# Performance work log

Hardware: AMD Instinct MI355X
Metric: run time of the kernel (lower is better)

Reference implementation:

```python
import jax, jax.numpy as jnp
import numpy as np

S = 17          # number of segment ids (0 = background, skipped)
MIN_H = 100.0   # HomographySmoothLoss.min_segment_pixels
MIN_V = 50.0    # ObjectVarianceLoss.min_segment_pixels
SUPPRESS = 0.1  # BoundaryAwareSmoothLoss.boundary_suppress


def _maxpool3(x):
    # torch F.max_pool2d(k=3, stride=1, pad=1) pads with -inf
    return jax.lax.reduce_window(x, -jnp.inf, jax.lax.max,
                                 (1, 1, 3, 3), (1, 1, 1, 1),
                                 ((0, 0), (0, 0), (1, 1), (1, 1)))


def _boundary_map(masks):
    lab = masks.astype(jnp.float32)[:, None]  # (B,1,H,W)
    dil = _maxpool3(lab)
    ero = -_maxpool3(-lab)
    return (dil != ero).astype(jnp.float32)


def _nearest(x, Ho, Wo):
    # torch F.interpolate(mode='nearest'): src = floor(dst * in/out)
    H, W = x.shape[-2], x.shape[-1]
    yi = (jnp.arange(Ho) * H) // Ho
    xi = (jnp.arange(Wo) * W) // Wo
    return x[..., yi, :][..., :, xi]


def _conv3(x, k):
    return jax.lax.conv_general_dilated(x, k, (1, 1), ((1, 1), (1, 1)),
                                        dimension_numbers=('NCHW', 'OIHW', 'NCHW'))


def _segment_losses(flow, masks):
    # Vectorized replacement of per-(batch,segment) python loops:
    # accumulate per-segment moments with segment_sum, then batched 3x3
    # normal-equation solves (equivalent to torch.lstsq affine fit).
    B, _, H, W = flow.shape
    NS = B * S
    xs = jnp.broadcast_to(jnp.arange(W, dtype=jnp.float32)[None, None, :], (B, H, W)).reshape(-1)
    ys = jnp.broadcast_to(jnp.arange(H, dtype=jnp.float32)[None, :, None], (B, H, W)).reshape(-1)
    u = flow[:, 0].reshape(-1)
    v = flow[:, 1].reshape(-1)
    seg = masks.reshape(-1)
    bidx = jnp.repeat(jnp.arange(B, dtype=jnp.int32), H * W)
    idx = bidx * S + seg                                  # global segment id
    ones = jnp.ones_like(xs)
    feats = jnp.stack([ones, xs, ys, xs * xs, xs * ys, ys * ys,
                       u, v, u * u, v * v, xs * u, ys * u, xs * v, ys * v], axis=1)
    sums = jax.ops.segment_sum(feats, idx, num_segments=NS)  # (NS,14)
    (n, Sx, Sy, Sxx, Sxy, Syy, Su, Sv, Suu, Svv,
     Sxu, Syu, Sxv, Syv) = [sums[:, i] for i in range(14)]
    segids = jnp.tile(jnp.arange(S), B)

    # ---- homography loss: per-segment affine least-squares fit ----
    valid_h = (segids != 0) & (n >= MIN_H)
    ATA = jnp.stack([jnp.stack([Sxx, Sxy, Sx], -1),
                     jnp.stack([Sxy, Syy, Sy], -1),
                     jnp.stack([Sx, Sy, n], -1)], axis=1)   # (NS,3,3)
    eye3 = jnp.eye(3, dtype=flow.dtype)
    ATA = jnp.where(valid_h[:, None, None], ATA, eye3)      # keep solve nonsingular
    ATb = jnp.stack([jnp.stack([Sxu, Sxv], -1),
                     jnp.stack([Syu, Syv], -1),
                     jnp.stack([Su, Sv], -1)], axis=1)      # (NS,3,2)
    ATb = jnp.where(valid_h[:, None, None], ATb, 0.0)
    params = jnp.linalg.solve(ATA, ATb)                     # (NS,3,2): [a,b,c] for u and v
    p = params[idx]                                         # (BHW,3,2) gather per pixel
    pred_u = xs * p[:, 0, 0] + ys * p[:, 1, 0] + p[:, 2, 0]
    pred_v = xs * p[:, 0, 1] + ys * p[:, 1, 1] + p[:, 2, 1]
    res = jnp.sqrt((u - pred_u) ** 2 + (v - pred_v) ** 2)
    res_mean = jax.ops.segment_sum(res, idx, num_segments=NS) / jnp.maximum(n, 1.0)
    nh = jnp.maximum(jnp.sum(valid_h), 1)
    homog = jnp.sum(res_mean * valid_h) / nh

    # ---- object variance loss (unbiased var, matches torch .var()) ----
    valid_v = (segids != 0) & (n >= MIN_V)
    nsafe = jnp.maximum(n, 2.0)
    var_u = (Suu - Su * Su / nsafe) / (nsafe - 1.0)
    var_v = (Svv - Sv * Sv / nsafe) / (nsafe - 1.0)
    nv = jnp.maximum(jnp.sum(valid_v), 1)
    ovar = jnp.sum((var_u + var_v) * valid_v) / nv
    return homog, ovar


def setup_inputs():
    key = jax.random.key(0)
    k1, k2, k3 = jax.random.split(key, 3)
    B, H, W = 8, 512, 1024
    flow = jax.random.normal(k1, (B, 2, H, W), jnp.float32)
    masks = jax.random.randint(k2, (B, H, W), 0, S).astype(jnp.int32)
    images = jax.random.uniform(k3, (B, 3, H, W), jnp.float32)
    return {"flow": flow, "masks": masks, "images": images}


def reference(flow, masks, images):
    boundary = _boundary_map(masks)                         # (B,1,H,W)
    homog, ovar = _segment_losses(flow, masks)

    # ---- boundary sharpness (sobel on flow magnitude) ----
    sobel_x = jnp.array([[-1., 0., 1.], [-2., 0., 2.], [-1., 0., 1.]], jnp.float32).reshape(1, 1, 3, 3)
    sobel_y = jnp.array([[-1., -2., -1.], [0., 0., 0.], [1., 2., 1.]], jnp.float32).reshape(1, 1, 3, 3)
    flow_mag = jnp.sqrt(jnp.sum(flow ** 2, axis=1, keepdims=True))
    fg = jnp.abs(_conv3(flow_mag, sobel_x)) + jnp.abs(_conv3(flow_mag, sobel_y))
    fg = fg / (jnp.max(fg) + 1e-6)
    bn = boundary / (jnp.max(boundary) + 1e-6)
    sharp = jnp.mean(bn * (1.0 - fg))

    # ---- boundary-aware edge-weighted smoothness ----
    flow_dx = flow[:, :, :, 1:] - flow[:, :, :, :-1]
    flow_dy = flow[:, :, 1:, :] - flow[:, :, :-1, :]
    g = jnp.mean(images, axis=1, keepdims=True)
    wx = jnp.exp(-jnp.abs(g[:, :, :, 1:] - g[:, :, :, :-1]) * 10.0)
    wy = jnp.exp(-jnp.abs(g[:, :, 1:, :] - g[:, :, :-1, :]) * 10.0)
    bx = _nearest(boundary, wx.shape[2], wx.shape[3])
    by = _nearest(boundary, wy.shape[2], wy.shape[3])
    wx = wx * (1.0 - (1.0 - SUPPRESS) * bx)
    wy = wy * (1.0 - (1.0 - SUPPRESS) * by)
    smooth = jnp.mean(jnp.abs(flow_dx) * wx) + jnp.mean(jnp.abs(flow_dy) * wy)

    # weights all 1.0; order: homography, boundary_sharpness, object_variance, boundary_smooth
    return jnp.stack([homog, sharp, ovar, smooth])
```

## Files before the change

kernel.cpp:

```cpp
#include <hip/hip_runtime.h>
#include <math.h>

#define BB 8
#define HH 512
#define WW 1024
#define HW (HH * WW)
#define NPIX (BB * HW)
#define NSEG 16
#define SUPPRESS 0.1f


__device__ __forceinline__ float wave_sum(float t) {
    #pragma unroll
    for (int off = 32; off > 0; off >>= 1) t += __shfl_down(t, off);
    return t;
}

#define REP8(M) M(0) M(1) M(2) M(3) M(4) M(5) M(6) M(7)


__device__ void moments_body(
    const float* __restrict__ flow, const int* __restrict__ masks,
    double* __restrict__ moments4, float* bins, int bid)
{
    const int tid  = threadIdx.x;
    const int lane = tid & 63;
    const int wid  = tid >> 6;
    const int colg = bid & 15;
    const int rowg = (bid >> 4) & 7;
    const int b    = bid >> 7;
    const int par  = bid & 3;

    const int c0 = colg * 64;
    const int r0 = rowg * 64;

    const float* fu = flow + (long long)b * (2LL * HW);
    const float* fv = fu + HW;
    const int*   mk = masks + (long long)b * HW;
    const int*   mrow = mk + r0 * WW + c0 + lane;
    const float* urow = fu + r0 * WW + c0 + lane;
    const float* vrow = fv + r0 * WW + c0 + lane;

    for (int i = tid; i < 2496; i += 256)
        *(float4*)&bins[i * 4] = make_float4(0.f, 0.f, 0.f, 0.f);
    __syncthreads();

    int   m0 = mrow[0];
    float u0 = urow[0], v0 = vrow[0];
    int   m1 = mrow[WW];
    float u1 = urow[WW], v1 = vrow[WW];

#define MPROC(RR, MM, UU, VV) { \
    const float y = (float)(r0 + (RR)); \
    float* bp = &bins[(MM) * 576 + lane]; \
    if (wid == 0) { \
        float b0 = bp[0], b1 = bp[64], b2 = bp[128]; \
        b0 += 1.f; b1 += y; b2 = fmaf(y, y, b2); \
        bp[0] = b0; bp[64] = b1; bp[128] = b2; \
    } else if (wid == 1) { \
        float b3 = bp[192], b5 = bp[320]; \
        b3 += (UU); b5 = fmaf((UU), (UU), b5); \
        bp[192] = b3; bp[320] = b5; \
    } else if (wid == 2) { \
        float b4 = bp[256], b6 = bp[384]; \
        b4 += (VV); b6 = fmaf((VV), (VV), b6); \
        bp[256] = b4; bp[384] = b6; \
    } else { \
        float b7 = bp[448], b8 = bp[512]; \
        b7 = fmaf(y, (UU), b7); b8 = fmaf(y, (VV), b8); \
        bp[448] = b7; bp[512] = b8; \
    } }

    #pragma unroll 1
    for (int r = 0; r < 64; r += 2) {
        const int o2 = ((r + 2) & 63) * WW;
        const int o3 = ((r + 3) & 63) * WW;
        const int   m2 = mrow[o2];
        const float u2 = urow[o2], v2 = vrow[o2];
        const int   m3 = mrow[o3];
        const float u3 = urow[o3], v3 = vrow[o3];

        MPROC(r, m0, u0, v0)
        MPROC(r + 1, m1, u1, v1)

        m0 = m2; u0 = u2; v0 = v2;
        m1 = m3; u1 = u3; v1 = v3;
    }
    __syncthreads();

    const unsigned long long SRC = 0x84736543210100ULL;
    const unsigned long long PW  = 0x01010000012010ULL;
    double* cell = moments4 + par * 1792 + b * 224;
    {
        const int p   = tid;
        const int act = (p < 224);
        const int pc  = act ? p : 0;
        const int segm = pc / 14;
        const int feat = pc - segm * 14;
        const int srcb = (int)((SRC >> (4 * feat)) & 15);
        const int pw   = (int)((PW  >> (4 * feat)) & 15);
        const float* bp = &bins[(segm + 1) * 576 + srcb * 64];
        float acc = 0.f;
        #pragma unroll 8
        for (int l0 = 0; l0 < 64; ++l0) {
            const int l = (l0 + lane) & 63;
            const float xv = (float)(c0 + l);
            const float w = (pw == 0) ? 1.f : ((pw == 1) ? xv : xv * xv);
            acc = fmaf(bp[l], w, acc);
        }
        if (act) atomicAdd(&cell[segm * 14 + feat], (double)acc);
    }
}

__device__ void stencil_body(
    const float* __restrict__ flow, const int* __restrict__ masks,
    const float* __restrict__ images,
    double* __restrict__ scal64, unsigned* __restrict__ maxfg64,
    char* smem, int bid)
{
    float    (*smX)[260] = (float (*)[260])(smem);
    float    (*smW)[260] = (float (*)[260])(smem + 4160);
    unsigned (*mX)[260]  = (unsigned (*)[260])(smem + 8320);
    unsigned (*mW)[260]  = (unsigned (*)[260])(smem + 12480);
    float    (*gX)[260]  = (float (*)[260])(smem + 16640);
    float    (*ue)[260]  = (float (*)[260])(smem + 18720);
    float    (*ve)[260]  = (float (*)[260])(smem + 20800);
    float    (*wred)[5]  = (float (*)[5])(smem + 22880);

    const int tid = threadIdx.x;
    const int lane = tid & 63;
    const long long base = (long long)bid * 2048;
    const int b  = (int)(base >> 19);
    const int h0 = (int)((base & (HW - 1)) >> 10);

    const float* fu = flow + (long long)b * (2LL * HW);
    const float* fv = fu + HW;
    const int*   mk = masks + (long long)b * HW;
    const float* i0 = images + (long long)b * (3LL * HW);
    const float* i1 = i0 + HW;
    const float* i2 = i1 + HW;

    const int c4 = tid * 4;
    float4 m4a[4];
    unsigned mbp[4];
    float4 ur[3], vr[3];
    float4 gr[3];

    #pragma unroll
    for (int r = 0; r < 4; ++r) {
        const int grow = h0 - 1 + r;
        const int mr = grow < 0 ? 0 : (grow > HH - 1 ? HH - 1 : grow);
        const int4 mv = *(const int4*)&mk[mr * WW + c4];
        mbp[r] = (unsigned)(mv.x & 255) | ((unsigned)(mv.y & 255) << 8) |
                 ((unsigned)(mv.z & 255) << 16) | ((unsigned)(mv.w & 255) << 24);

        float4 u4 = make_float4(0.f, 0.f, 0.f, 0.f);
        float4 v4 = make_float4(0.f, 0.f, 0.f, 0.f);
        if (grow >= 0 && grow <= HH - 1) {
            u4 = *(const float4*)&fu[grow * WW + c4];
            v4 = *(const float4*)&fv[grow * WW + c4];
        }
        float4 m4;
        m4.x = sqrtf(u4.x * u4.x + v4.x * v4.x);
        m4.y = sqrtf(u4.y * u4.y + v4.y * v4.y);
        m4.z = sqrtf(u4.z * u4.z + v4.z * v4.z);
        m4.w = sqrtf(u4.w * u4.w + v4.w * v4.w);
        m4a[r] = m4;
        smX[r][tid] = m4.x;
        smW[r][tid + 1] = m4.w;
        mX[r][tid] = (unsigned)(mv.x & 255);
        mW[r][tid + 1] = (unsigned)(mv.w & 255);
        if (tid == 0)   { smW[r][0] = 0.f;   mW[r][0] = (unsigned)(mv.x & 255); }
        if (tid == 255) { smX[r][256] = 0.f; mX[r][256] = (unsigned)(mv.w & 255); }
        if (r >= 1) { ur[r - 1] = u4; vr[r - 1] = v4; }
    }
    #pragma unroll
    for (int r = 0; r < 3; ++r) {
        const int grow = h0 + r;
        float4 g4 = make_float4(0.f, 0.f, 0.f, 0.f);
        if (grow <= HH - 1) {
            const float4 a  = *(const float4*)&i0[grow * WW + c4];
            const float4 bq = *(const float4*)&i1[grow * WW + c4];
            const float4 c  = *(const float4*)&i2[grow * WW + c4];
            g4.x = (a.x + bq.x + c.x) * (1.f / 3.f);
            g4.y = (a.y + bq.y + c.y) * (1.f / 3.f);
            g4.z = (a.z + bq.z + c.z) * (1.f / 3.f);
            g4.w = (a.w + bq.w + c.w) * (1.f / 3.f);
        }
        gr[r] = g4;
        if (r < 2) gX[r][tid] = g4.x;
    }
    ue[0][tid] = ur[0].x; ve[0][tid] = vr[0].x;
    ue[1][tid] = ur[1].x; ve[1][tid] = vr[1].x;
    __syncthreads();

    float a_dx = 0.f, a_dy = 0.f, a_sb = 0.f, a_sbf = 0.f, mfg = 0.f;

    #pragma unroll
    for (int lr = 0; lr < 2; ++lr) {
        const int h = h0 + lr;
        float a[3][6];
        unsigned long long kw[3];
        #pragma unroll
        for (int r = 0; r < 3; ++r) {
            const int rr = lr + r;
            const float4 own = m4a[rr];
            a[r][0] = smW[rr][tid];
            a[r][1] = own.x; a[r][2] = own.y; a[r][3] = own.z; a[r][4] = own.w;
            a[r][5] = smX[rr][tid + 1];
            kw[r] = (unsigned long long)mW[rr][tid]
                  | ((unsigned long long)mbp[rr] << 8)
                  | ((unsigned long long)mX[rr][tid + 1] << 40);
        }
        const float4 gc = gr[lr];
        const float4 gd4 = gr[lr + 1];
        const float gval[5] = {gc.x, gc.y, gc.z, gc.w, gX[lr][tid + 1]};
        const float gd[4]  = {gd4.x, gd4.y, gd4.z, gd4.w};
        const float4 uc4 = ur[lr],  vc4 = vr[lr];
        const float4 ud4 = ur[lr + 1], vd4 = vr[lr + 1];
        const float uc[5] = {uc4.x, uc4.y, uc4.z, uc4.w, ue[lr][tid + 1]};
        const float vc[5] = {vc4.x, vc4.y, vc4.z, vc4.w, ve[lr][tid + 1]};
        const float ud[4] = {ud4.x, ud4.y, ud4.z, ud4.w};
        const float vd[4] = {vd4.x, vd4.y, vd4.z, vd4.w};

        #pragma unroll
        for (int j = 0; j < 4; ++j) {
            const int w = c4 + j;
            const unsigned cseg = (unsigned)((kw[1] >> (8 * (j + 1))) & 255);
            int bnd = (((kw[0] >> (8 * j)) & 255) != cseg)
                    | (((kw[0] >> (8 * (j + 1))) & 255) != cseg)
                    | (((kw[0] >> (8 * (j + 2))) & 255) != cseg)
                    | (((kw[1] >> (8 * j)) & 255) != cseg)
                    | (((kw[1] >> (8 * (j + 2))) & 255) != cseg)
                    | (((kw[2] >> (8 * j)) & 255) != cseg)
                    | (((kw[2] >> (8 * (j + 1))) & 255) != cseg)
                    | (((kw[2] >> (8 * (j + 2))) & 255) != cseg);

            const float fgx = (a[0][j + 2] - a[0][j]) + 2.f * (a[1][j + 2] - a[1][j]) +
                              (a[2][j + 2] - a[2][j]);
            const float fgy = (a[2][j] + 2.f * a[2][j + 1] + a[2][j + 2]) -
                              (a[0][j] + 2.f * a[0][j + 1] + a[0][j + 2]);
            const float fgraw = fabsf(fgx) + fabsf(fgy);
            mfg = fmaxf(mfg, fgraw);
            if (bnd) { a_sb += 1.f; a_sbf += fgraw; }

            const float u = uc[j], v = vc[j], g0 = gval[j];
            if (w < WW - 1) {
                const float wgt = expf(-fabsf(gval[j + 1] - g0) * 10.f) * (bnd ? SUPPRESS : 1.f);
                a_dx += (fabsf(uc[j + 1] - u) + fabsf(vc[j + 1] - v)) * wgt;
            }
            if (h < HH - 1) {
                const float wgt = expf(-fabsf(gd[j] - g0) * 10.f) * (bnd ? SUPPRESS : 1.f);
                a_dy += (fabsf(ud[j] - u) + fabsf(vd[j] - v)) * wgt;
            }
        }
    }

    for (int off = 32; off > 0; off >>= 1) {
        a_dx += __shfl_down(a_dx, off);
        a_dy += __shfl_down(a_dy, off);
        a_sb += __shfl_down(a_sb, off);
        a_sbf += __shfl_down(a_sbf, off);
        mfg = fmaxf(mfg, __shfl_down(mfg, off));
    }
    if (lane == 0) {
        const int wv = tid >> 6;
        wred[wv][0] = a_dx; wred[wv][1] = a_dy; wred[wv][2] = a_sb;
        wred[wv][3] = a_sbf; wred[wv][4] = mfg;
    }
    __syncthreads();
    if (tid == 0) {
        float dx = 0.f, dy = 0.f, sb = 0.f, sbf = 0.f, mf = 0.f;
        for (int i = 0; i < 4; ++i) {
            dx += wred[i][0]; dy += wred[i][1]; sb += wred[i][2];
            sbf += wred[i][3]; mf = fmaxf(mf, wred[i][4]);
        }
        const int sl = bid & 63;
        atomicAdd(&scal64[sl * 4 + 0], (double)dx);
        atomicAdd(&scal64[sl * 4 + 1], (double)dy);
        atomicAdd(&scal64[sl * 4 + 2], (double)sb);
        atomicAdd(&scal64[sl * 4 + 3], (double)sbf);
        atomicMax(&maxfg64[sl], __float_as_uint(mf));
    }
}

__global__ __launch_bounds__(256) void uber_kernel(
    const float* __restrict__ flow,
    const int*   __restrict__ masks,
    const float* __restrict__ images,
    double* __restrict__ moments4,
    double* __restrict__ scal64,
    unsigned* __restrict__ maxfg64)
{
    __shared__ char smem[39936];
    const int bid = blockIdx.x;
    if ((bid % 3) == 2) {
        moments_body(flow, masks, moments4, (float*)smem, bid / 3);
    } else {
        stencil_body(flow, masks, images, scal64, maxfg64, smem,
                     (bid / 3) * 2 + (bid % 3));
    }
}

__global__ __launch_bounds__(128) void solve_kernel(
    const double* __restrict__ moments4,
    float* __restrict__ params,
    int* __restrict__ valid,
    float* __restrict__ out)
{
    const int i = threadIdx.x;
    double m[14];
    #pragma unroll
    for (int k = 0; k < 14; ++k) {
        double s = 0.0;
        #pragma unroll
        for (int par = 0; par < 4; ++par) s += moments4[par * 1792 + i * 14 + k];
        m[k] = s;
    }
    const double n = m[0];
    const int vh = (n >= 100.0) ? 1 : 0;
    float p[6] = {0.f, 0.f, 0.f, 0.f, 0.f, 0.f};
    if (vh) {
        double A[3][3] = {{m[3], m[4], m[1]},
                          {m[4], m[5], m[2]},
                          {m[1], m[2], n}};
        double Bm[3][2] = {{m[10], m[12]},
                           {m[11], m[13]},
                           {m[6],  m[7]}};
        for (int k = 0; k < 3; ++k) {
            int piv = k; double mx = fabs(A[k][k]);
            for (int r = k + 1; r < 3; ++r) {
                double a = fabs(A[r][k]);
                if (a > mx) { mx = a; piv = r; }
            }
            if (piv != k) {
                for (int c = 0; c < 3; ++c) { double t = A[k][c]; A[k][c] = A[piv][c]; A[piv][c] = t; }
                for (int c = 0; c < 2; ++c) { double t = Bm[k][c]; Bm[k][c] = Bm[piv][c]; Bm[piv][c] = t; }
            }
            const double inv = 1.0 / A[k][k];
            for (int r = k + 1; r < 3; ++r) {
                const double f = A[r][k] * inv;
                for (int c = k; c < 3; ++c) A[r][c] -= f * A[k][c];
                Bm[r][0] -= f * Bm[k][0];
                Bm[r][1] -= f * Bm[k][1];
            }
        }
        double X[3][2];
        for (int c = 0; c < 2; ++c) {
            X[2][c] = Bm[2][c] / A[2][2];
            X[1][c] = (Bm[1][c] - A[1][2] * X[2][c]) / A[1][1];
            X[0][c] = (Bm[0][c] - A[0][1] * X[1][c] - A[0][2] * X[2][c]) / A[0][0];
        }
        p[0] = (float)X[0][0]; p[1] = (float)X[1][0]; p[2] = (float)X[2][0];
        p[3] = (float)X[0][1]; p[4] = (float)X[1][1]; p[5] = (float)X[2][1];
    }
    valid[i] = vh;
    for (int c = 0; c < 6; ++c) params[i * 6 + c] = p[c];

    const int vv = (n >= 50.0) ? 1 : 0;
    double var = 0.0;
    if (vv) {
        const double ns = (n > 2.0) ? n : 2.0;
        const double var_u = (m[8] - m[6] * m[6] / ns) / (ns - 1.0);
        const double var_v = (m[9] - m[7] * m[7] / ns) / (ns - 1.0);
        var = var_u + var_v;
    }
    __shared__ double svar[128];
    __shared__ int scnt[128];
    svar[i] = var; scnt[i] = vv;
    __syncthreads();
    for (int s = 64; s > 0; s >>= 1) {
        if (i < s) { svar[i] += svar[i + s]; scnt[i] += scnt[i + s]; }
        __syncthreads();
    }
    if (i == 0) out[2] = (float)(svar[0] / (double)(scnt[0] > 1 ? scnt[0] : 1));
}

__global__ __launch_bounds__(256) void pass2_kernel(
    const float* __restrict__ flow,
    const int*   __restrict__ masks,
    const float* __restrict__ params,
    double* __restrict__ res4)
{
    __shared__ float sp[17 * 6];

    const long long base = (long long)blockIdx.x * 4096;
    const int b      = (int)(base >> 19);
    const int hwbase = (int)(base & (HW - 1));
    const int tid    = threadIdx.x;
    const int lane   = tid & 63;

    if (tid < 6) sp[tid] = 0.f;
    if (tid < 96) sp[6 + tid] = params[b * 96 + tid];
    __syncthreads();

    const float* fu = flow + (long long)b * (2LL * HW);
    const float* fv = fu + HW;
    const int*   mk = masks + (long long)b * HW;

#define DECLR(i) float r_##i = 0.f;
    REP8(DECLR)
#define DECLR2(i) float q_##i = 0.f;
    REP8(DECLR2)

    #pragma unroll
    for (int it = 0; it < 4; ++it) {
        const int i4 = hwbase + it * 1024 + tid * 4;
        const int4   m4 = *(const int4*)&mk[i4];
        const float4 u4 = *(const float4*)&fu[i4];
        const float4 v4 = *(const float4*)&fv[i4];
        const int segs[4] = {m4.x, m4.y, m4.z, m4.w};
        const float us[4] = {u4.x, u4.y, u4.z, u4.w};
        const float vs[4] = {v4.x, v4.y, v4.z, v4.w};
        #pragma unroll
        for (int j = 0; j < 4; ++j) {
            const int seg = segs[j];
            const float* pf = &sp[seg * 6];
            const int hw = i4 + j;
            const float x = (float)(hw & 1023), y = (float)((hw & (HW - 1)) >> 10);
            const float du = us[j] - (x * pf[0] + y * pf[1] + pf[2]);
            const float dv = vs[j] - (x * pf[3] + y * pf[4] + pf[5]);
            const float r = sqrtf(du * du + dv * dv);
            const int sr = seg - 1;
#define STEPR(i) r_##i += (sr == i) ? r : 0.f;
            REP8(STEPR)
#define STEPR2(i) q_##i += (sr == 8 + i) ? r : 0.f;
            REP8(STEPR2)
        }
    }

    const int par = blockIdx.x & 3;
    double* rb = &res4[par * 128 + b * 16];
#define FINR(i) { const float s = wave_sum(r_##i); \
    if (lane == 0) atomicAdd(rb + i, (double)s); }
    REP8(FINR)
#define FINR2(i) { const float s = wave_sum(q_##i); \
    if (lane == 0) atomicAdd(rb + 8 + i, (double)s); }
    REP8(FINR2)
}

__global__ __launch_bounds__(128) void final_kernel(
    const double* __restrict__ moments4,
    const double* __restrict__ res4,
    const int*    __restrict__ valid,
    const double* __restrict__ scal64,
    const unsigned* __restrict__ maxfg64,
    float* __restrict__ out)
{
    const int i = threadIdx.x;
    double n = 0.0, rs = 0.0;
    #pragma unroll
    for (int par = 0; par < 4; ++par) {
        n  += moments4[par * 1792 + i * 14];
        rs += res4[par * 128 + i];
    }
    const int vh = valid[i];
    const double rm = vh ? rs / (n > 1.0 ? n : 1.0) : 0.0;
    __shared__ double sr[128];
    __shared__ int sc[128];
    sr[i] = rm; sc[i] = vh;
    __syncthreads();
    for (int s = 64; s > 0; s >>= 1) {
        if (i < s) { sr[i] += sr[i + s]; sc[i] += sc[i + s]; }
        __syncthreads();
    }
    if (i == 0) {
        out[0] = (float)(sr[0] / (double)(sc[0] > 1 ? sc[0] : 1));
        double dx = 0.0, dy = 0.0, sb = 0.0, sbf = 0.0;
        float mf = 0.f;
        for (int k = 0; k < 64; ++k) {
            dx += scal64[k * 4 + 0]; dy += scal64[k * 4 + 1];
            sb += scal64[k * 4 + 2]; sbf += scal64[k * 4 + 3];
            mf = fmaxf(mf, __uint_as_float(maxfg64[k]));
        }
        const double maxfg = (double)mf;
        const double maxb = (sb > 0.0) ? 1.0 : 0.0;
        out[1] = (float)((sb - sbf / (maxfg + 1e-6)) / (maxb + 1e-6) / (double)NPIX);
        const double smooth = dx / (double)(2LL * BB * HH * (WW - 1)) +
                              dy / (double)(2LL * BB * (HH - 1) * WW);
        out[3] = (float)smooth;
    }
}

extern "C" void kernel_launch(void* const* d_in, const int* in_sizes, int n_in,
                              void* d_out, int out_size, void* d_ws, size_t ws_size,
                              hipStream_t stream)
{
    const float* flow   = (const float*)d_in[0];
    const int*   masks  = (const int*)d_in[1];
    const float* images = (const float*)d_in[2];
    float* out = (float*)d_out;

    char* ws = (char*)d_ws;
    double*   moments4 = (double*)(ws);
    double*   res4     = (double*)(ws + 57344);
    double*   scal64   = (double*)(ws + 61440);
    unsigned* maxfg64  = (unsigned*)(ws + 63488);
    float*    params   = (float*)(ws + 63744);
    int*      valid    = (int*)(ws + 66816);

    hipMemsetAsync(d_ws, 0, 67584, stream);

    uber_kernel<<<dim3(3072), dim3(256), 0, stream>>>(
        flow, masks, images, moments4, scal64, maxfg64);
    solve_kernel<<<dim3(1), dim3(128), 0, stream>>>(moments4, params, valid, out);
    pass2_kernel<<<dim3(NPIX / 4096), dim3(256), 0, stream>>>(
        flow, masks, params, res4);
    final_kernel<<<dim3(1), dim3(128), 0, stream>>>(
        moments4, res4, valid, scal64, maxfg64, out);
}
```

Before: 106.5 us.

## Split moment accumulation into u-only and v-only blocks to shrink LDS

The per-tile moment accumulation block is split into two block types. One handles the u channel (y, y², u, u², yu bins) and the other the v channel (count, v, v², yv bins). Each uses a smaller shared-memory histogram, so the uber kernel's static LDS drops from about 39 KB to about 23 KB, which should allow more resident blocks per CU. It also cuts per-block LDS read-modify-write work. The grid grows from 3072 to 4096 blocks, and the mask is now read twice, once by each moments block.

```diff
diff --git a/kernel.cpp b/kernel.cpp
--- a/kernel.cpp
+++ b/kernel.cpp
@@ -19,7 +19,7 @@
 #define REP8(M) M(0) M(1) M(2) M(3) M(4) M(5) M(6) M(7)
 
 
-__device__ void moments_body(
+__device__ void momentsA_body(
     const float* __restrict__ flow, const int* __restrict__ masks,
     double* __restrict__ moments4, float* bins, int bid)
 {
@@ -35,71 +35,69 @@
     const int r0 = rowg * 64;
 
     const float* fu = flow + (long long)b * (2LL * HW);
-    const float* fv = fu + HW;
     const int*   mk = masks + (long long)b * HW;
     const int*   mrow = mk + r0 * WW + c0 + lane;
     const float* urow = fu + r0 * WW + c0 + lane;
-    const float* vrow = fv + r0 * WW + c0 + lane;
-
-    for (int i = tid; i < 2496; i += 256)
+
+    for (int i = tid; i < 1360; i += 256)
         *(float4*)&bins[i * 4] = make_float4(0.f, 0.f, 0.f, 0.f);
     __syncthreads();
 
     int   m0 = mrow[0];
-    float u0 = urow[0], v0 = vrow[0];
+    float u0 = urow[0];
     int   m1 = mrow[WW];
-    float u1 = urow[WW], v1 = vrow[WW];
-
-#define MPROC(RR, MM, UU, VV) { \
-    const float y = (float)(r0 + (RR)); \
-    float* bp = &bins[(MM) * 576 + lane]; \
-    if (wid == 0) { \
-        float b0 = bp[0], b1 = bp[64], b2 = bp[128]; \
-        b0 += 1.f; b1 += y; b2 = fmaf(y, y, b2); \
-        bp[0] = b0; bp[64] = b1; bp[128] = b2; \
-    } else if (wid == 1) { \
-        float b3 = bp[192], b5 = bp[320]; \
-        b3 += (UU); b5 = fmaf((UU), (UU), b5); \
-        bp[192] = b3; bp[320] = b5; \
-    } else if (wid == 2) { \
-        float b4 = bp[256], b6 = bp[384]; \
-        b4 += (VV); b6 = fmaf((VV), (VV), b6); \
-        bp[256] = b4; bp[384] = b6; \
-    } else { \
-        float b7 = bp[448], b8 = bp[512]; \
-        b7 = fmaf(y, (UU), b7); b8 = fmaf(y, (VV), b8); \
-        bp[448] = b7; bp[512] = b8; \
-    } }
+    float u1 = urow[WW];
 
     #pragma unroll 1
     for (int r = 0; r < 64; r += 2) {
         const int o2 = ((r + 2) & 63) * WW;
         const int o3 = ((r + 3) & 63) * WW;
         const int   m2 = mrow[o2];
-        const float u2 = urow[o2], v2 = vrow[o2];
+        const float u2 = urow[o2];
         const int   m3 = mrow[o3];
-        const float u3 = urow[o3], v3 = vrow[o3];
-
-        MPROC(r, m0, u0, v0)
-        MPROC(r + 1, m1, u1, v1)
-
-        m0 = m2; u0 = u2; v0 = v2;
-        m1 = m3; u1 = u3; v1 = v3;
-    }
-    __syncthreads();
-
-    const unsigned long long SRC = 0x84736543210100ULL;
-    const unsigned long long PW  = 0x01010000012010ULL;
+        const float u3 = urow[o3];
+
+        {
+            const float y = (float)(r0 + r);
+            float* bp = &bins[m0 * 320 + lane];
+            if (wid == 0) {
+                float s0 = bp[0], s1 = bp[64];
+                s0 += y; s1 = fmaf(y, y, s1);
+                bp[0] = s0; bp[64] = s1;
+            } else if (wid == 1) { bp[128] += u0; }
+            else if (wid == 2)   { bp[192] = fmaf(u0, u0, bp[192]); }
+            else                 { bp[256] = fmaf(y, u0, bp[256]); }
+        }
+        {
+            const float y = (float)(r0 + r + 1);
+            float* bp = &bins[m1 * 320 + lane];
+            if (wid == 0) {
+                float s0 = bp[0], s1 = bp[64];
+                s0 += y; s1 = fmaf(y, y, s1);
+                bp[0] = s0; bp[64] = s1;
+            } else if (wid == 1) { bp[128] += u1; }
+            else if (wid == 2)   { bp[192] = fmaf(u1, u1, bp[192]); }
+            else                 { bp[256] = fmaf(y, u1, bp[256]); }
+        }
+        m0 = m2; u0 = u2;
+        m1 = m3; u1 = u3;
+    }
+    __syncthreads();
+
+    const unsigned SRC = 0x4232100u;
+    const unsigned PW  = 0x0100010u;
+    const unsigned DST = 0xBA86542u;
     double* cell = moments4 + par * 1792 + b * 224;
     {
         const int p   = tid;
-        const int act = (p < 224);
+        const int act = (p < 112);
         const int pc  = act ? p : 0;
-        const int segm = pc / 14;
-        const int feat = pc - segm * 14;
-        const int srcb = (int)((SRC >> (4 * feat)) & 15);
-        const int pw   = (int)((PW  >> (4 * feat)) & 15);
-        const float* bp = &bins[(segm + 1) * 576 + srcb * 64];
+        const int segm = pc / 7;
+        const int k    = pc - segm * 7;
+        const int srcb = (int)((SRC >> (4 * k)) & 15);
+        const int pw   = (int)((PW  >> (4 * k)) & 15);
+        const int dst  = (int)((DST >> (4 * k)) & 15);
+        const float* bp = &bins[(segm + 1) * 320 + srcb * 64];
         float acc = 0.f;
         #pragma unroll 8
         for (int l0 = 0; l0 < 64; ++l0) {
@@ -108,7 +106,92 @@
             const float w = (pw == 0) ? 1.f : ((pw == 1) ? xv : xv * xv);
             acc = fmaf(bp[l], w, acc);
         }
-        if (act) atomicAdd(&cell[segm * 14 + feat], (double)acc);
+        if (act) atomicAdd(&cell[segm * 14 + dst], (double)acc);
+    }
+}
+
+__device__ void momentsB_body(
+    const float* __restrict__ flow, const int* __restrict__ masks,
+    double* __restrict__ moments4, float* bins, int bid)
+{
+    const int tid  = threadIdx.x;
+    const int lane = tid & 63;
+    const int wid  = tid >> 6;
+    const int colg = bid & 15;
+    const int rowg = (bid >> 4) & 7;
+    const int b    = bid >> 7;
+    const int par  = bid & 3;
+
+    const int c0 = colg * 64;
+    const int r0 = rowg * 64;
+
+    const float* fv = flow + (long long)b * (2LL * HW) + HW;
+    const int*   mk = masks + (long long)b * HW;
+    const int*   mrow = mk + r0 * WW + c0 + lane;
+    const float* vrow = fv + r0 * WW + c0 + lane;
+
+    for (int i = tid; i < 1088; i += 256)
+        *(float4*)&bins[i * 4] = make_float4(0.f, 0.f, 0.f, 0.f);
+    __syncthreads();
+
+    int   m0 = mrow[0];
+    float v0 = vrow[0];
+    int   m1 = mrow[WW];
+    float v1 = vrow[WW];
+
+    #pragma unroll 1
+    for (int r = 0; r < 64; r += 2) {
+        const int o2 = ((r + 2) & 63) * WW;
+        const int o3 = ((r + 3) & 63) * WW;
+        const int   m2 = mrow[o2];
+        const float v2 = vrow[o2];
+        const int   m3 = mrow[o3];
+        const float v3 = vrow[o3];
+
+        {
+            const float y = (float)(r0 + r);
+            float* bp = &bins[m0 * 256 + lane];
+            if (wid == 0)      { bp[0] += 1.f; }
+            else if (wid == 1) { bp[64] += v0; }
+            else if (wid == 2) { bp[128] = fmaf(v0, v0, bp[128]); }
+            else               { bp[192] = fmaf(y, v0, bp[192]); }
+        }
+        {
+            const float y = (float)(r0 + r + 1);
+            float* bp = &bins[m1 * 256 + lane];
+            if (wid == 0)      { bp[0] += 1.f; }
+            else if (wid == 1) { bp[64] += v1; }
+            else if (wid == 2) { bp[128] = fmaf(v1, v1, bp[128]); }
+            else               { bp[192] = fmaf(y, v1, bp[192]); }
+        }
+        m0 = m2; v0 = v2;
+        m1 = m3; v1 = v3;
+    }
+    __syncthreads();
+
+    const unsigned SRC = 0x3121000u;
+    const unsigned PW  = 0x0100210u;
+    const unsigned DST = 0xDC97310u;
+    double* cell = moments4 + par * 1792 + b * 224;
+    {
+        const int p   = tid;
+        const int act = (p < 112);
+        const int pc  = act ? p : 0;
+        const int segm = pc / 7;
+        const int k    = pc - segm * 7;
+        const int srcb = (int)((SRC >> (4 * k)) & 15);
+        const int pw   = (int)((PW  >> (4 * k)) & 15);
+        const int dst  = (int)((DST >> (4 * k)) & 15);
+        const float* bp = &bins[(segm + 1) * 256 + srcb * 64];
+        float acc = 0.f;
+        #pragma unroll 8
+        for (int l0 = 0; l0 < 64; ++l0) {
+            const int l = (l0 + lane) & 63;
+            const float xv = (float)(c0 + l);
+            const float w = (pw == 0) ? 1.f : ((pw == 1) ? xv : xv * xv);
+            acc = fmaf(bp[l], w, acc);
+        }
+        if (act) atomicAdd(&cell[segm * 14 + dst], (double)acc);
     }
 }
 
@@ -292,13 +375,14 @@
     double* __restrict__ scal64,
     unsigned* __restrict__ maxfg64)
 {
-    __shared__ char smem[39936];
+    __shared__ __align__(16) char smem[23040];
     const int bid = blockIdx.x;
-    if ((bid % 3) == 2) {
-        moments_body(flow, masks, moments4, (float*)smem, bid / 3);
+    if ((bid & 1) == 0) {
+        stencil_body(flow, masks, images, scal64, maxfg64, smem, bid >> 1);
+    } else if ((bid & 3) == 1) {
+        momentsA_body(flow, masks, moments4, (float*)smem, bid >> 2);
     } else {
-        stencil_body(flow, masks, images, scal64, maxfg64, smem,
-                     (bid / 3) * 2 + (bid % 3));
+        momentsB_body(flow, masks, moments4, (float*)smem, bid >> 2);
     }
 }
 
@@ -501,7 +585,7 @@
 
     hipMemsetAsync(d_ws, 0, 67584, stream);
 
-    uber_kernel<<<dim3(3072), dim3(256), 0, stream>>>(
+    uber_kernel<<<dim3(4096), dim3(256), 0, stream>>>(
         flow, masks, images, moments4, scal64, maxfg64);
     solve_kernel<<<dim3(1), dim3(128), 0, stream>>>(moments4, params, valid, out);
     pass2_kernel<<<dim3(NPIX / 4096), dim3(256), 0, stream>>>(
```

Measured after the change: 128.5 us. +20.6%, slower.
